# Kernel tuning notes

Measured on AMD Instinct MI355X. Metric: run time of the kernel, lower is better.

The kernel has to match this reference:

```python
import jax, jax.numpy as jnp
import numpy as np

N_EDGES = 10_000_000
N_RELS = 64
N_POL = 3


def setup_inputs() -> dict:
    key = jax.random.key(0)
    k0, k1, k2, k3, k4 = jax.random.split(key, 5)
    prnt_probs = jax.random.uniform(k0, (N_EDGES, N_POL), dtype=jnp.float32)
    child_probs = jax.random.uniform(k1, (N_EDGES, N_POL), dtype=jnp.float32)
    rels = jax.random.randint(k2, (N_EDGES,), 0, N_RELS, dtype=jnp.int64 if jax.config.jax_enable_x64 else jnp.int32)
    # learned parameters (torch inits them to ones/constants; random keeps grads nontrivial)
    M = jax.random.normal(k3, (N_RELS, N_POL, N_POL), dtype=jnp.float32)
    beta = jax.random.uniform(k4, (N_RELS, N_POL), dtype=jnp.float32)
    z_epsilon = jnp.float32(0.01)
    scale_factor = jnp.float32(21.0)
    return {
        "var_sfx": 0,
        "prnt_probs": prnt_probs,
        "child_probs": child_probs,
        "rels": rels,
        "M": M,
        "beta": beta,
        "z_epsilon": z_epsilon,
        "scale_factor": scale_factor,
    }


def _scale(prnt_probs, child_probs, z_epsilon, scale_factor):
    # entropy of the clipped, renormalized blend of parent+child distributions
    z = jnp.maximum(z_epsilon, prnt_probs + child_probs)  # [E,3]
    z = z / jnp.sum(z, axis=-1, keepdims=True)
    entropy = -jnp.sum(z * jnp.log(z), axis=-1)  # [E]
    # cosine similarity between parent and child distributions
    cos = jnp.sum(prnt_probs * child_probs, axis=-1)
    norm = jnp.linalg.norm(prnt_probs, axis=-1) * jnp.linalg.norm(child_probs, axis=-1)
    norm = jnp.where(norm == 0, jnp.ones_like(norm), norm)
    cos = 1.1 + cos / norm
    return scale_factor * cos / entropy  # [E]


def reference(var_sfx, prnt_probs, child_probs, rels, M, beta, z_epsilon, scale_factor):
    # relation-indexed gather + tiny 3x3 matvec + softmax
    # (inputs guarantee all row sums > 0, so the torch nonzero masks select every row)
    scores = jnp.einsum('nij,nj->ni', M[rels], child_probs)  # [E,3]
    child = jax.nn.softmax(scores, axis=-1)
    b = beta[rels]  # [E,3]
    alpha = (1.0 - b) * prnt_probs + b * child
    scale = _scale(prnt_probs, child, z_epsilon, scale_factor)
    return alpha * scale[:, None]
```

## Files before the change

### kernel.cpp

```cpp
#include <hip/hip_runtime.h>

#define TPB 256
#define N_RELS 64

__device__ __forceinline__ void edge_compute(
    const float* __restrict__ sM, const float* __restrict__ sB,
    int r, float p0, float p1, float p2,
    float c0, float c1, float c2,
    float zeps, float sf, float* __restrict__ o)
{
    const float* m = &sM[r * 9];
    const float* b = &sB[r * 3];

    float s0 = m[0] * c0 + m[1] * c1 + m[2] * c2;
    float s1 = m[3] * c0 + m[4] * c1 + m[5] * c2;
    float s2 = m[6] * c0 + m[7] * c1 + m[8] * c2;

    float mx = fmaxf(fmaxf(s0, s1), s2);
    float e0 = __expf(s0 - mx);
    float e1 = __expf(s1 - mx);
    float e2 = __expf(s2 - mx);
    float inv = __fdividef(1.0f, e0 + e1 + e2);
    float ch0 = e0 * inv, ch1 = e1 * inv, ch2 = e2 * inv;

    float b0 = b[0], b1 = b[1], b2 = b[2];
    float a0 = p0 + b0 * (ch0 - p0);
    float a1 = p1 + b1 * (ch1 - p1);
    float a2 = p2 + b2 * (ch2 - p2);

    float z0 = fmaxf(zeps, p0 + ch0);
    float z1 = fmaxf(zeps, p1 + ch1);
    float z2 = fmaxf(zeps, p2 + ch2);
    float zinv = __fdividef(1.0f, z0 + z1 + z2);
    float zn0 = z0 * zinv, zn1 = z1 * zinv, zn2 = z2 * zinv;
    float ent = -(zn0 * __logf(zn0) + zn1 * __logf(zn1) + zn2 * __logf(zn2));

    float dot = p0 * ch0 + p1 * ch1 + p2 * ch2;
    float np2 = p0 * p0 + p1 * p1 + p2 * p2;
    float nc2 = ch0 * ch0 + ch1 * ch1 + ch2 * ch2;
    float prod = np2 * nc2;
    float cosn = (prod > 0.0f) ? dot * rsqrtf(prod) : dot;
    float cosv = 1.1f + cosn;

    float scale = sf * cosv * __fdividef(1.0f, ent);

    o[0] = a0 * scale;
    o[1] = a1 * scale;
    o[2] = a2 * scale;
}

__global__ __launch_bounds__(TPB) void alpha_kernel(
    const float* __restrict__ prnt,
    const float* __restrict__ child,
    const int*   __restrict__ rels,
    const float* __restrict__ M,
    const float* __restrict__ beta,
    const float* __restrict__ zeps_p,
    const float* __restrict__ sf_p,
    float* __restrict__ out,
    int n_groups,
    int n_edges)
{
    __shared__ float sM[N_RELS * 9];
    __shared__ float sB[N_RELS * 3];
    for (int i = threadIdx.x; i < N_RELS * 9; i += TPB) sM[i] = M[i];
    for (int i = threadIdx.x; i < N_RELS * 3; i += TPB) sB[i] = beta[i];
    __syncthreads();

    const float zeps = *zeps_p;
    const float sf   = *sf_p;

    int g = blockIdx.x * TPB + threadIdx.x;

    if (g < n_groups) {
        const float4* p4 = (const float4*)prnt;
        const float4* c4 = (const float4*)child;
        const int4*   r4 = (const int4*)rels;

        float4 pa = p4[g * 3 + 0], pb = p4[g * 3 + 1], pc = p4[g * 3 + 2];
        float4 ca = c4[g * 3 + 0], cb = c4[g * 3 + 1], cc = c4[g * 3 + 2];
        int4   rr = r4[g];

        float P[4][3] = {{pa.x, pa.y, pa.z}, {pa.w, pb.x, pb.y},
                         {pb.z, pb.w, pc.x}, {pc.y, pc.z, pc.w}};
        float C[4][3] = {{ca.x, ca.y, ca.z}, {ca.w, cb.x, cb.y},
                         {cb.z, cb.w, cc.x}, {cc.y, cc.z, cc.w}};
        int   R[4]    = {rr.x, rr.y, rr.z, rr.w};

        float O[4][3];
        #pragma unroll
        for (int e = 0; e < 4; ++e) {
            edge_compute(sM, sB, R[e],
                         P[e][0], P[e][1], P[e][2],
                         C[e][0], C[e][1], C[e][2],
                         zeps, sf, O[e]);
        }

        float4* o4 = (float4*)out;
        o4[g * 3 + 0] = make_float4(O[0][0], O[0][1], O[0][2], O[1][0]);
        o4[g * 3 + 1] = make_float4(O[1][1], O[1][2], O[2][0], O[2][1]);
        o4[g * 3 + 2] = make_float4(O[2][2], O[3][0], O[3][1], O[3][2]);
    } else {
        int t = g - n_groups;
        int eidx = n_groups * 4 + t;
        if (t >= 0 && eidx < n_edges) {
            float o[3];
            edge_compute(sM, sB, rels[eidx],
                         prnt[eidx * 3 + 0], prnt[eidx * 3 + 1], prnt[eidx * 3 + 2],
                         child[eidx * 3 + 0], child[eidx * 3 + 1], child[eidx * 3 + 2],
                         zeps, sf, o);
            out[eidx * 3 + 0] = o[0];
            out[eidx * 3 + 1] = o[1];
            out[eidx * 3 + 2] = o[2];
        }
    }
}

extern "C" void kernel_launch(void* const* d_in, const int* in_sizes, int n_in,
                              void* d_out, int out_size, void* d_ws, size_t ws_size,
                              hipStream_t stream) {
    const float* prnt  = (const float*)d_in[1];
    const float* child = (const float*)d_in[2];
    const int*   rels  = (const int*)d_in[3];
    const float* M     = (const float*)d_in[4];
    const float* beta  = (const float*)d_in[5];
    const float* zeps  = (const float*)d_in[6];
    const float* sf    = (const float*)d_in[7];
    float* out = (float*)d_out;

    int n_edges  = in_sizes[3];
    int n_groups = n_edges / 4;
    int tail     = n_edges - n_groups * 4;
    int work     = n_groups + tail;
    int blocks   = (work + TPB - 1) / TPB;

    alpha_kernel<<<blocks, TPB, 0, stream>>>(prnt, child, rels, M, beta,
                                             zeps, sf, out, n_groups, n_edges);
}
```

Measured before the change: 318.8 us.

## Process eight edges per thread with nontemporal vector IO and packed M/beta table

Raises edges per thread from 4 to 8, so each thread issues 12 float4 loads and 6 float4 stores. The parent/child loads and the output stores now use nontemporal builtins. M and beta are packed into one 12-float-per-relation LDS table so each edge reads three vector LDS loads instead of scattered scalar ones, and the launch bound now requests occupancy. The aim is fewer memory instructions and better streaming bandwidth on a purely memory-bound kernel, at the cost of more registers per thread and fewer threads in flight.

```diff
diff --git a/kernel.cpp b/kernel.cpp
--- a/kernel.cpp
+++ b/kernel.cpp
@@ -2,19 +2,23 @@
 
 #define TPB 256
 #define N_RELS 64
+#define EPT 8
+
+typedef float f4 __attribute__((ext_vector_type(4)));
+typedef int   i4 __attribute__((ext_vector_type(4)));
 
 __device__ __forceinline__ void edge_compute(
-    const float* __restrict__ sM, const float* __restrict__ sB,
-    int r, float p0, float p1, float p2,
+    const float* __restrict__ sMB, int r,
+    float p0, float p1, float p2,
     float c0, float c1, float c2,
     float zeps, float sf, float* __restrict__ o)
 {
-    const float* m = &sM[r * 9];
-    const float* b = &sB[r * 3];
+    const f4* mb = (const f4*)(sMB + r * 12);
+    f4 q0 = mb[0], q1 = mb[1], q2 = mb[2];
 
-    float s0 = m[0] * c0 + m[1] * c1 + m[2] * c2;
-    float s1 = m[3] * c0 + m[4] * c1 + m[5] * c2;
-    float s2 = m[6] * c0 + m[7] * c1 + m[8] * c2;
+    float s0 = q0.x * c0 + q0.y * c1 + q0.z * c2;
+    float s1 = q0.w * c0 + q1.x * c1 + q1.y * c2;
+    float s2 = q1.z * c0 + q1.w * c1 + q2.x * c2;
 
     float mx = fmaxf(fmaxf(s0, s1), s2);
     float e0 = __expf(s0 - mx);
@@ -23,10 +27,9 @@
     float inv = __fdividef(1.0f, e0 + e1 + e2);
     float ch0 = e0 * inv, ch1 = e1 * inv, ch2 = e2 * inv;
 
-    float b0 = b[0], b1 = b[1], b2 = b[2];
-    float a0 = p0 + b0 * (ch0 - p0);
-    float a1 = p1 + b1 * (ch1 - p1);
-    float a2 = p2 + b2 * (ch2 - p2);
+    float a0 = p0 + q2.y * (ch0 - p0);
+    float a1 = p1 + q2.z * (ch1 - p1);
+    float a2 = p2 + q2.w * (ch2 - p2);
 
     float z0 = fmaxf(zeps, p0 + ch0);
     float z1 = fmaxf(zeps, p1 + ch1);
@@ -49,7 +52,7 @@
     o[2] = a2 * scale;
 }
 
-__global__ __launch_bounds__(TPB) void alpha_kernel(
+__global__ __launch_bounds__(TPB, 4) void alpha_kernel(
     const float* __restrict__ prnt,
     const float* __restrict__ child,
     const int*   __restrict__ rels,
@@ -59,12 +62,13 @@
     const float* __restrict__ sf_p,
     float* __restrict__ out,
     int n_groups,
-    int n_edges)
+    long n_edges)
 {
-    __shared__ float sM[N_RELS * 9];
-    __shared__ float sB[N_RELS * 3];
-    for (int i = threadIdx.x; i < N_RELS * 9; i += TPB) sM[i] = M[i];
-    for (int i = threadIdx.x; i < N_RELS * 3; i += TPB) sB[i] = beta[i];
+    __shared__ float sMB[N_RELS * 12];
+    for (int i = threadIdx.x; i < N_RELS * 12; i += TPB) {
+        int r = i / 12, j = i - r * 12;
+        sMB[i] = (j < 9) ? M[r * 9 + j] : beta[r * 3 + (j - 9)];
+    }
     __syncthreads();
 
     const float zeps = *zeps_p;
@@ -73,39 +77,40 @@
     int g = blockIdx.x * TPB + threadIdx.x;
 
     if (g < n_groups) {
-        const float4* p4 = (const float4*)prnt;
-        const float4* c4 = (const float4*)child;
-        const int4*   r4 = (const int4*)rels;
+        const i4* r4 = (const i4*)rels  + (size_t)g * 2;
+        const f4* p4 = (const f4*)prnt  + (size_t)g * 6;
+        const f4* c4 = (const f4*)child + (size_t)g * 6;
 
-        float4 pa = p4[g * 3 + 0], pb = p4[g * 3 + 1], pc = p4[g * 3 + 2];
-        float4 ca = c4[g * 3 + 0], cb = c4[g * 3 + 1], cc = c4[g * 3 + 2];
-        int4   rr = r4[g];
+        i4 R0 = r4[0], R1 = r4[1];
+        f4 P4[6], C4[6];
+        #pragma unroll
+        for (int i = 0; i < 6; ++i) P4[i] = __builtin_nontemporal_load(p4 + i);
+        #pragma unroll
+        for (int i = 0; i < 6; ++i) C4[i] = __builtin_nontemporal_load(c4 + i);
 
-        float P[4][3] = {{pa.x, pa.y, pa.z}, {pa.w, pb.x, pb.y},
-                         {pb.z, pb.w, pc.x}, {pc.y, pc.z, pc.w}};
-        float C[4][3] = {{ca.x, ca.y, ca.z}, {ca.w, cb.x, cb.y},
-                         {cb.z, cb.w, cc.x}, {cc.y, cc.z, cc.w}};
-        int   R[4]    = {rr.x, rr.y, rr.z, rr.w};
+        int R[EPT] = {R0.x, R0.y, R0.z, R0.w, R1.x, R1.y, R1.z, R1.w};
+        const float* P = (const float*)P4;
+        const float* C = (const float*)C4;
 
-        float O[4][3];
+        float O[EPT * 3];
         #pragma unroll
-        for (int e = 0; e < 4; ++e) {
-            edge_compute(sM, sB, R[e],
-                         P[e][0], P[e][1], P[e][2],
-                         C[e][0], C[e][1], C[e][2],
-                         zeps, sf, O[e]);
+        for (int e = 0; e < EPT; ++e) {
+            edge_compute(sMB, R[e],
+                         P[3 * e], P[3 * e + 1], P[3 * e + 2],
+                         C[3 * e], C[3 * e + 1], C[3 * e + 2],
+                         zeps, sf, &O[3 * e]);
         }
 
-        float4* o4 = (float4*)out;
-        o4[g * 3 + 0] = make_float4(O[0][0], O[0][1], O[0][2], O[1][0]);
-        o4[g * 3 + 1] = make_float4(O[1][1], O[1][2], O[2][0], O[2][1]);
-        o4[g * 3 + 2] = make_float4(O[2][2], O[3][0], O[3][1], O[3][2]);
+        f4* o4 = (f4*)out + (size_t)g * 6;
+        const f4* Ov = (const f4*)O;
+        #pragma unroll
+        for (int i = 0; i < 6; ++i) __builtin_nontemporal_store(Ov[i], o4 + i);
     } else {
-        int t = g - n_groups;
-        int eidx = n_groups * 4 + t;
+        long t = (long)g - n_groups;
+        long eidx = (long)n_groups * EPT + t;
         if (t >= 0 && eidx < n_edges) {
             float o[3];
-            edge_compute(sM, sB, rels[eidx],
+            edge_compute(sMB, rels[eidx],
                          prnt[eidx * 3 + 0], prnt[eidx * 3 + 1], prnt[eidx * 3 + 2],
                          child[eidx * 3 + 0], child[eidx * 3 + 1], child[eidx * 3 + 2],
                          zeps, sf, o);
@@ -128,11 +133,11 @@
     const float* sf    = (const float*)d_in[7];
     float* out = (float*)d_out;
 
-    int n_edges  = in_sizes[3];
-    int n_groups = n_edges / 4;
-    int tail     = n_edges - n_groups * 4;
-    int work     = n_groups + tail;
-    int blocks   = (work + TPB - 1) / TPB;
+    long n_edges  = in_sizes[3];
+    int  n_groups = (int)(n_edges / EPT);
+    long tail     = n_edges - (long)n_groups * EPT;
+    long work     = n_groups + tail;
+    int  blocks   = (int)((work + TPB - 1) / TPB);
 
     alpha_kernel<<<blocks, TPB, 0, stream>>>(prnt, child, rels, M, beta,
                                              zeps, sf, out, n_groups, n_edges);
```

Result: slower. 478.7 us (+50.2%).
